# Kernel tuning notes

Measured on AMD Instinct MI355X. Metric: run time of the kernel, lower is better.

Reference implementation:

```python
import jax, jax.numpy as jnp
import numpy as np

B = 8192          # batch of scenes
H = 20            # human_num
O = 10            # other_robot_num
IN = 13           # input_dim
SELF = 6          # self_state_dim
AG = IN - SELF    # agent_state_dim = 7
E1, E2 = 256, 128 # wr_dims / wh_dims
HID = 32          # hardcoded hidden_channels in Graphgnn
FIN = 128         # final_state_dim
P1, P2, P3 = 256, 128, 1  # planning_dims
NE = 8            # number of hetero edge types
# edge-type index convention:
# 0 robot->human, 1 human->robot, 2 other->robot, 3 robot->other,
# 4 other->human, 5 human->other, 6 human->human, 7 other->other


def setup_inputs() -> dict:
    key = jax.random.key(0)
    ks = iter(jax.random.split(key, 40))
    def nrm(shape, scale=0.05):
        return jax.random.normal(next(ks), shape, jnp.float32) * scale
    inp = {}
    inp["state"] = jax.random.normal(next(ks), (B, H + O, IN), jnp.float32)
    inp["dropout"] = 0  # unused by forward (kept for signature fidelity)
    # w_r: SELF -> E1 -> E2 (last_relu=True)
    inp["wr_W0"] = nrm((SELF, E1)); inp["wr_b0"] = nrm((E1,))
    inp["wr_W1"] = nrm((E1, E2));   inp["wr_b1"] = nrm((E2,))
    # w_h: AG -> E1 -> E2
    inp["wh_W0"] = nrm((AG, E1));   inp["wh_b0"] = nrm((E1,))
    inp["wh_W1"] = nrm((E1, E2));   inp["wh_b1"] = nrm((E2,))
    # w_o: AG -> E1 -> E2
    inp["wo_W0"] = nrm((AG, E1));   inp["wo_b0"] = nrm((E1,))
    inp["wo_W1"] = nrm((E1, E2));   inp["wo_b1"] = nrm((E2,))
    # per-edge-type GraphConv params (PyG GraphConv: lin_rel has bias, lin_root has none)
    inp["c1_relW"]  = nrm((NE, E2, HID)); inp["c1_relb"]  = nrm((NE, HID))
    inp["c1_rootW"] = nrm((NE, E2, HID))
    inp["c2_relW"]  = nrm((NE, HID, FIN)); inp["c2_relb"]  = nrm((NE, FIN))
    inp["c2_rootW"] = nrm((NE, HID, FIN))
    # value_net: FIN -> P1 -> P2 -> P3 (no final relu)
    inp["v_W0"] = nrm((FIN, P1)); inp["v_b0"] = nrm((P1,))
    inp["v_W1"] = nrm((P1, P2));  inp["v_b1"] = nrm((P2,))
    inp["v_W2"] = nrm((P2, P3));  inp["v_b2"] = nrm((P3,))
    return inp


def _mlp2(x, W0, b0, W1, b1, last_relu):
    h = jax.nn.relu(x @ W0 + b0)
    h = h @ W1 + b1
    return jax.nn.relu(h) if last_relu else h


def _hetero_conv(xr, xh, xo, relW, relb, rootW):
    # xr: [B,1,D], xh: [B,H,D], xo: [B,O,D]
    # GraphConv per edge type: out_dst = lin_root(x_dst) + lin_rel(sum of src messages)
    # graph is complete bipartite (sence) / complete-minus-self (affect),
    # so aggregations are closed-form sums.
    lin  = lambda x, i: jnp.einsum('bnd,do->bno', x, relW[i]) + relb[i]
    root = lambda x, i: jnp.einsum('bnd,do->bno', x, rootW[i])
    sh = xh.sum(axis=1, keepdims=True)  # [B,1,D] sum over humans
    so = xo.sum(axis=1, keepdims=True)  # [B,1,D] sum over other robots
    # robot receives: human->robot (1), other->robot (2)
    out_r = lin(sh, 1) + root(xr, 1) + lin(so, 2) + root(xr, 2)
    # human receives: robot->human (0), other->human (4), human->human (6)
    out_h = (lin(xr, 0) + root(xh, 0)
             + lin(so, 4) + root(xh, 4)
             + lin(sh - xh, 6) + root(xh, 6))
    # other receives: robot->other (3), human->other (5), other->other (7)
    out_o = (lin(xr, 3) + root(xo, 3)
             + lin(sh, 5) + root(xo, 5)
             + lin(so - xo, 7) + root(xo, 7))
    return out_r, out_h, out_o


def reference(state, dropout,
              wr_W0, wr_b0, wr_W1, wr_b1,
              wh_W0, wh_b0, wh_W1, wh_b1,
              wo_W0, wo_b0, wo_W1, wo_b1,
              c1_relW, c1_relb, c1_rootW,
              c2_relW, c2_relb, c2_rootW,
              v_W0, v_b0, v_W1, v_b1, v_W2, v_b2):
    self_state = state[:, 0, :SELF]          # [B, SELF]
    human_states = state[:, :H, SELF:]       # [B, H, AG]
    other_states = state[:, H:, SELF:]       # [B, O, AG]
    er = _mlp2(self_state, wr_W0, wr_b0, wr_W1, wr_b1, True)[:, None, :]  # [B,1,E2]
    eh = _mlp2(human_states, wh_W0, wh_b0, wh_W1, wh_b1, True)            # [B,H,E2]
    eo = _mlp2(other_states, wo_W0, wo_b0, wo_W1, wo_b1, True)            # [B,O,E2]
    r, h, o = _hetero_conv(er, eh, eo, c1_relW, c1_relb, c1_rootW)
    r, h, o = jax.nn.relu(r), jax.nn.relu(h), jax.nn.relu(o)
    r, h, o = _hetero_conv(r, h, o, c2_relW, c2_relb, c2_rootW)
    r = jax.nn.relu(r)
    hr = r[:, 0, :]                           # robot node per scene, [B, FIN]
    v = jax.nn.relu(hr @ v_W0 + v_b0)
    v = jax.nn.relu(v @ v_W1 + v_b1)
    v = v @ v_W2 + v_b2                       # [B, 1]
    return v
```

## Files before the change

kernel.cpp:

```cpp
#include <hip/hip_runtime.h>
#include <hip/hip_bf16.h>
#include <stdint.h>

#define BATCH 8192
#define NSTATE 30
#define DIN 13
#define E1 256
#define E2 128

typedef short bf16x8 __attribute__((ext_vector_type(8)));
typedef float f32x4 __attribute__((ext_vector_type(4)));

__device__ __forceinline__ unsigned short f2b(float f) {
    unsigned u = __float_as_uint(f);
    u += 0x7FFFu + ((u >> 16) & 1u);
    return (unsigned short)(u >> 16);
}
__device__ __forceinline__ float b2f(unsigned short b) {
    return __uint_as_float((unsigned)b << 16);
}
__device__ __forceinline__ unsigned pack2(float a, float b) {
    return ((unsigned)f2b(fmaxf(b, 0.f)) << 16) | f2b(fmaxf(a, 0.f));
}
__device__ __forceinline__ unsigned pack2n(float a, float b) {
    return ((unsigned)f2b(b) << 16) | f2b(a);
}

__device__ __forceinline__ float wcat_val(int k, int m, const float* relW, const float* rootW) {
    int part = k >> 7, c = k & 127, grp = m >> 5, mm = m & 31;
    int off = c * 32 + mm;
    if (part == 0) return (grp == 0) ? rootW[4096 + off] + rootW[8192 + off]
                        : (grp == 1) ? relW[off] : relW[3*4096 + off];
    if (part == 1) return (grp == 0) ? relW[1*4096 + off]
                        : (grp == 1) ? relW[6*4096 + off] : relW[5*4096 + off];
    return (grp == 0) ? relW[2*4096 + off]
         : (grp == 1) ? relW[4*4096 + off] : relW[7*4096 + off];
}
__device__ __forceinline__ float wc2_val(int k, int n, const float* relW, const float* rootW) {
    int grp = k >> 5, kk = k & 31;
    int off = kk * 128 + n;
    if (grp == 0) return rootW[4096 + off] + rootW[8192 + off];
    if (grp == 1) return relW[4096 + off];
    return relW[8192 + off];
}

__global__ void k_prep(const float* __restrict__ c1_relW, const float* __restrict__ c1_relb,
                       const float* __restrict__ c1_rootW,
                       const float* __restrict__ c2_relW, const float* __restrict__ c2_relb,
                       const float* __restrict__ c2_rootW,
                       const float* __restrict__ wh_W0, const float* __restrict__ wh_W1,
                       const float* __restrict__ wo_W0, const float* __restrict__ wo_W1,
                       const float* __restrict__ wr_W0, const float* __restrict__ wr_W1,
                       const float* __restrict__ v_W0, const float* __restrict__ v_W1,
                       float* __restrict__ bcat, float* __restrict__ bc2,
                       unsigned short* __restrict__ W0b_h, unsigned short* __restrict__ W0b_o,
                       unsigned short* __restrict__ W0b_r,
                       unsigned short* __restrict__ W1f_h, unsigned short* __restrict__ W1f_o,
                       unsigned short* __restrict__ W1f_r,
                       unsigned short* __restrict__ Mf_h, unsigned short* __restrict__ Mf_o,
                       unsigned short* __restrict__ Wcatf, unsigned short* __restrict__ Wc2f,
                       unsigned short* __restrict__ vW0f, unsigned short* __restrict__ vW1f)
{
    int gid = blockIdx.x * blockDim.x + threadIdx.x;
    int gsz = gridDim.x * blockDim.x;

    for (int i = gid; i < 96; i += gsz) {
        int grp = i >> 5, mm = i & 31;
        float v;
        if (grp == 0)      v = c1_relb[32 + mm] + c1_relb[64 + mm];
        else if (grp == 1) v = c1_relb[mm] + c1_relb[128 + mm] + c1_relb[192 + mm];
        else               v = c1_relb[96 + mm] + c1_relb[160 + mm] + c1_relb[224 + mm];
        bcat[i] = v;
    }
    for (int i = gid; i < 128; i += gsz) bc2[i] = c2_relb[128 + i] + c2_relb[256 + i];

    for (int i = gid; i < 2048; i += gsz) {
        int n = i >> 3, j = i & 7;
        W0b_h[i] = (j < 7) ? f2b(wh_W0[j * 256 + n]) : 0;
        W0b_o[i] = (j < 7) ? f2b(wo_W0[j * 256 + n]) : 0;
        W0b_r[i] = (j < 6) ? f2b(wr_W0[j * 256 + n]) : 0;
    }
    for (int i = gid; i < 32768; i += gsz) {
        int j = i & 7, l = (i >> 3) & 63, nt = (i >> 9) & 7, ks = i >> 12;
        int k = ks * 32 + (l >> 4) * 8 + j;
        int n = nt * 16 + (l & 15);
        W1f_h[i] = f2b(wh_W1[k * 128 + n]);
        W1f_o[i] = f2b(wo_W1[k * 128 + n]);
        W1f_r[i] = f2b(wr_W1[k * 128 + n]);
    }
    for (int i = gid; i < 4096; i += gsz) {
        int j = i & 7, l = (i >> 3) & 63, nt = (i >> 9) & 1, ks = i >> 10;
        int k = ks * 32 + (l >> 4) * 8 + j;
        int n = nt * 16 + (l & 15);
        int i0 = k * 32 + n;
        Mf_h[i] = f2b(c1_rootW[i0] + c1_rootW[4*4096 + i0] + c1_rootW[6*4096 + i0] - c1_relW[6*4096 + i0]);
        Mf_o[i] = f2b(c1_rootW[3*4096 + i0] + c1_rootW[5*4096 + i0] + c1_rootW[7*4096 + i0] - c1_relW[7*4096 + i0]);
    }
    for (int i = gid; i < 36864; i += gsz) {
        int j = i & 7, l = (i >> 3) & 63, rem = i >> 9;
        int nt = rem % 6, ks = rem / 6;
        int k = ks * 32 + (l >> 4) * 8 + j;
        int n = nt * 16 + (l & 15);
        Wcatf[i] = f2b(wcat_val(k, n, c1_relW, c1_rootW));
    }
    for (int i = gid; i < 12288; i += gsz) {
        int j = i & 7, l = (i >> 3) & 63, rem = i >> 9;
        int nt = rem & 7, ks = rem >> 3;
        int k = ks * 32 + (l >> 4) * 8 + j;
        int n = nt * 16 + (l & 15);
        Wc2f[i] = f2b(wc2_val(k, n, c2_relW, c2_rootW));
    }
    for (int i = gid; i < 32768; i += gsz) {
        int j = i & 7, l = (i >> 3) & 63, rem = i >> 9;
        int nt = rem & 15, ks = rem >> 4;
        int k = ks * 32 + (l >> 4) * 8 + j;
        int n = nt * 16 + (l & 15);
        vW0f[i] = f2b(v_W0[k * 256 + n]);
    }
    for (int i = gid; i < 32768; i += gsz) {
        int j = i & 7, l = (i >> 3) & 63, rem = i >> 9;
        int nt = rem & 7, ks = rem >> 3;
        int k = ks * 32 + (l >> 4) * 8 + j;
        int n = nt * 16 + (l & 15);
        vW1f[i] = f2b(v_W1[k * 128 + n]);
    }
}

#define SM_W0   0
#define SM_MF   4096
#define SM_W1   12288
#define SM_B0   77824
#define SM_B1   78848
#define SM_HS   79360
#define SM_SZ   (79360 + 8 * 16 * 264 * 2)

template<int NPB, int NODE0, int INOFF, int INDIM, bool TAIL>
__device__ __forceinline__ void mlp_blockE(
    int blkrow0, const float* __restrict__ state,
    const unsigned short* __restrict__ W0b_g, const float* __restrict__ b0,
    const unsigned short* __restrict__ W1f_g, const float* __restrict__ b1,
    const unsigned short* __restrict__ Mf_g,
    unsigned short* __restrict__ tR, float* __restrict__ sumB,
    unsigned short* __restrict__ eR, char* smem)
{
    unsigned short* W0s = (unsigned short*)(smem + SM_W0);
    unsigned short* Mfs = (unsigned short*)(smem + SM_MF);
    unsigned short* W1s = (unsigned short*)(smem + SM_W1);
    float* b0s          = (float*)(smem + SM_B0);
    float* b1s          = (float*)(smem + SM_B1);

    const int t = threadIdx.x;
    const int lane = t & 63;
    const int w = t >> 6;
    const int l15 = lane & 15;
    const int quad = lane >> 4;
    const int R0 = blkrow0 + w * 128;
    unsigned short* hw = (unsigned short*)(smem + SM_HS) + w * (16 * 264);
    unsigned short* ew = hw;

    if (t < 256) { ((uint4*)W0s)[t] = ((const uint4*)W0b_g)[t]; b0s[t] = b0[t]; }
    if (t >= 256 && t < 384) b1s[t - 256] = b1[t - 256];
    #pragma unroll
    for (int i = 0; i < 8; ++i)
        ((uint4*)W1s)[t + 512 * i] = ((const uint4*)W1f_g)[t + 512 * i];
    if constexpr (TAIL)
        ((uint4*)Mfs)[t] = ((const uint4*)Mf_g)[t];
    __syncthreads();

    float s0 = 0.f, s1 = 0.f;
    int bcur = R0 / NPB;

    for (int sub = 0; sub < 8; ++sub) {
        const int wrow0 = R0 + sub * 16;

        bf16x8 bx = {};
        if (quad == 0) {
            int grow = wrow0 + l15;
            int b = grow / NPB;
            int n = grow - b * NPB + NODE0;
            const float* xp = state + ((size_t)b * NSTATE + n) * DIN + INOFF;
            #pragma unroll
            for (int j = 0; j < INDIM; ++j)
                bx[j] = (short)f2b(xp[j]);
        }

        #pragma unroll
        for (int nt = 0; nt < 16; ++nt) {
            bf16x8 aw = {};
            if (quad == 0)
                aw = *(const bf16x8*)(W0s + (nt * 16 + l15) * 8);
            float4 bb = *(const float4*)(b0s + nt * 16 + quad * 4);
            f32x4 c = {bb.x, bb.y, bb.z, bb.w};
            c = __builtin_amdgcn_mfma_f32_16x16x32_bf16(aw, bx, c, 0, 0, 0);
            uint2 pv = {pack2(c[0], c[1]), pack2(c[2], c[3])};
            *(uint2*)(hw + l15 * 264 + nt * 16 + quad * 4) = pv;
        }

        f32x4 acc[8];
        #pragma unroll
        for (int nt = 0; nt < 8; ++nt) {
            float4 bb = *(const float4*)(b1s + nt * 16 + quad * 4);
            acc[nt] = (f32x4){bb.x, bb.y, bb.z, bb.w};
        }
        #pragma unroll
        for (int ks = 0; ks < 8; ++ks) {
            bf16x8 bh = *(const bf16x8*)(hw + l15 * 264 + ks * 32 + quad * 8);
            #pragma unroll
            for (int nt = 0; nt < 8; ++nt) {
                bf16x8 aw = *(const bf16x8*)(W1s + ((ks * 8 + nt) * 64 + lane) * 8);
                acc[nt] = __builtin_amdgcn_mfma_f32_16x16x32_bf16(aw, bh, acc[nt], 0, 0, 0);
            }
        }

        if constexpr (TAIL) {
            __asm__ __volatile__("s_waitcnt lgkmcnt(0)" ::: "memory");
            #pragma unroll
            for (int nt = 0; nt < 8; ++nt) {
                uint2 pv = {pack2(acc[nt][0], acc[nt][1]), pack2(acc[nt][2], acc[nt][3])};
                *(uint2*)(ew + l15 * 136 + nt * 16 + quad * 4) = pv;
            }

            f32x4 tacc[2] = {{0.f,0.f,0.f,0.f},{0.f,0.f,0.f,0.f}};
            #pragma unroll
            for (int ks = 0; ks < 4; ++ks) {
                bf16x8 ae = *(const bf16x8*)(ew + l15 * 136 + ks * 32 + quad * 8);
                #pragma unroll
                for (int nt = 0; nt < 2; ++nt) {
                    bf16x8 bm = *(const bf16x8*)(Mfs + ((ks * 2 + nt) * 64 + lane) * 8);
                    tacc[nt] = __builtin_amdgcn_mfma_f32_16x16x32_bf16(bm, ae, tacc[nt], 0, 0, 0);
                }
            }
            #pragma unroll
            for (int nt = 0; nt < 2; ++nt) {
                uint2 pv = {pack2n(tacc[nt][0], tacc[nt][1]), pack2n(tacc[nt][2], tacc[nt][3])};
                *(uint2*)(tR + (size_t)(wrow0 + l15) * 32 + nt * 16 + quad * 4) = pv;
            }

            #pragma unroll
            for (int r = 0; r < 16; ++r) {
                int b = (wrow0 + r) / NPB;
                if (b != bcur) {
                    bool interior = (bcur * NPB >= R0) && ((bcur + 1) * NPB <= R0 + 128);
                    float* dst = sumB + (size_t)bcur * 128 + 2 * lane;
                    if (interior) { dst[0] = s0; dst[1] = s1; }
                    else { atomicAdd(dst, s0); atomicAdd(dst + 1, s1); }
                    s0 = 0.f; s1 = 0.f; bcur = b;
                }
                unsigned v = *(const unsigned*)(ew + r * 136 + lane * 2);
                s0 += b2f((unsigned short)v);
                s1 += b2f((unsigned short)(v >> 16));
            }
            if (sub == 7) {
                bool interior = (bcur * NPB >= R0) && ((bcur + 1) * NPB <= R0 + 128);
                float* dst = sumB + (size_t)bcur * 128 + 2 * lane;
                if (interior) { dst[0] = s0; dst[1] = s1; }
                else { atomicAdd(dst, s0); atomicAdd(dst + 1, s1); }
            }
        } else {
            #pragma unroll
            for (int nt = 0; nt < 8; ++nt) {
                uint2 pv = {pack2(acc[nt][0], acc[nt][1]), pack2(acc[nt][2], acc[nt][3])};
                *(uint2*)(eR + (size_t)(wrow0 + l15) * 128 + nt * 16 + quad * 4) = pv;
            }
        }
        __asm__ __volatile__("" ::: "memory");
    }
}

__global__ __launch_bounds__(512, 2) void k_mlpE(
    const float* __restrict__ state,
    const unsigned short* __restrict__ W0b_h, const float* __restrict__ b0_h,
    const unsigned short* __restrict__ W1f_h, const float* __restrict__ b1_h,
    const unsigned short* __restrict__ Mf_h, unsigned short* __restrict__ tR_h,
    float* __restrict__ shB,
    const unsigned short* __restrict__ W0b_o, const float* __restrict__ b0_o,
    const unsigned short* __restrict__ W1f_o, const float* __restrict__ b1_o,
    const unsigned short* __restrict__ Mf_o, unsigned short* __restrict__ tR_o,
    float* __restrict__ soB,
    const unsigned short* __restrict__ W0b_r, const float* __restrict__ b0_r,
    const unsigned short* __restrict__ W1f_r, const float* __restrict__ b1_r,
    unsigned short* __restrict__ eR)
{
    __shared__ __align__(16) char smem[SM_SZ];
    int bid = blockIdx.x;
    if (bid < 160)
        mlp_blockE<20, 0, 6, 7, true>(bid * 1024, state, W0b_h, b0_h, W1f_h, b1_h,
                                      Mf_h, tR_h, shB, nullptr, smem);
    else if (bid < 240)
        mlp_blockE<10, 20, 6, 7, true>((bid - 160) * 1024, state, W0b_o, b0_o, W1f_o, b1_o,
                                       Mf_o, tR_o, soB, nullptr, smem);
    else
        mlp_blockE<1, 0, 0, 6, false>((bid - 240) * 1024, state, W0b_r, b0_r, W1f_r, b1_r,
                                      nullptr, nullptr, nullptr, eR, smem);
}

__global__ __launch_bounds__(256, 2) void k_tail(
    const unsigned short* __restrict__ eR,
    const float* __restrict__ shB, const float* __restrict__ soB,
    const unsigned short* __restrict__ tR_h, const unsigned short* __restrict__ tR_o,
    const unsigned short* __restrict__ Wcatf, const float* __restrict__ bcat,
    const unsigned short* __restrict__ Wc2f, const float* __restrict__ bc2,
    const unsigned short* __restrict__ vW0f, const float* __restrict__ vb0,
    const unsigned short* __restrict__ vW1f, const float* __restrict__ vb1,
    const float* __restrict__ vW2, const float* __restrict__ vb2,
    float* __restrict__ out)
{
    __shared__ __align__(16) char sm[33024];
    unsigned short* Ub  = (unsigned short*)(sm);
    unsigned short* V1b = (unsigned short*)(sm);
    unsigned short* Vb  = (unsigned short*)(sm + 12800);
    float* chL          = (float*)(sm + 16128);
    float* coL          = (float*)(sm + 18176);
    unsigned short* Hb  = (unsigned short*)(sm + 20224);
    float* V2b          = (float*)(sm + 24576);

    const int t = threadIdx.x, lane = t & 63, w = t >> 6;
    const int l15 = lane & 15, quad = lane >> 4;
    const int b0 = blockIdx.x * 16;
    const int rowb = quad * 4;

    {
        int b = t >> 4, q = t & 15;
        ((uint4*)(Ub + b * 400))[q] = ((const uint4*)(eR + (size_t)(b0 + b) * 128))[q];
    }
    for (int idx = t; idx < 4096; idx += 256) {
        int b = idx >> 8, kk = idx & 255;
        float v = (kk < 128) ? shB[(size_t)(b0 + b) * 128 + kk]
                             : soB[(size_t)(b0 + b) * 128 + kk - 128];
        Ub[b * 400 + 128 + kk] = f2b(v);
    }
    __syncthreads();

    for (int nt = w; nt < 6; nt += 4) {
        float bias = bcat[nt * 16 + l15];
        f32x4 acc = {bias, bias, bias, bias};
        #pragma unroll
        for (int ks = 0; ks < 12; ++ks) {
            bf16x8 a = *(const bf16x8*)(Ub + l15 * 400 + ks * 32 + quad * 8);
            bf16x8 bw = *(const bf16x8*)(Wcatf + ((ks * 6 + nt) * 64 + lane) * 8);
            acc = __builtin_amdgcn_mfma_f32_16x16x32_bf16(a, bw, acc, 0, 0, 0);
        }
        int n = nt * 16 + l15;
        #pragma unroll
        for (int reg = 0; reg < 4; ++reg) {
            float v = acc[reg];
            int b = rowb + reg;
            if (n < 32)      Vb[b * 104 + n] = f2b(fmaxf(v, 0.f));
            else if (n < 64) chL[b * 32 + (n - 32)] = v;
            else             coL[b * 32 + (n - 64)] = v;
        }
    }
    __syncthreads();

    for (int idx = t; idx < 512; idx += 256) {
        int b = idx >> 5, m = idx & 31;
        float ch = chL[b * 32 + m];
        const unsigned short* p = tR_h + (size_t)(b0 + b) * 20 * 32 + m;
        float s = 0.f;
        #pragma unroll
        for (int n = 0; n < 20; ++n) s += fmaxf(ch + b2f(p[n * 32]), 0.f);
        Vb[b * 104 + 32 + m] = f2b(s);
        float co = coL[b * 32 + m];
        const unsigned short* p2 = tR_o + (size_t)(b0 + b) * 10 * 32 + m;
        float s2 = 0.f;
        #pragma unroll
        for (int n = 0; n < 10; ++n) s2 += fmaxf(co + b2f(p2[n * 32]), 0.f);
        Vb[b * 104 + 64 + m] = f2b(s2);
    }
    __syncthreads();

    {
        f32x4 acc[2];
        #pragma unroll
        for (int q = 0; q < 2; ++q) {
            int nt = w + q * 4;
            float bias = bc2[nt * 16 + l15];
            acc[q] = (f32x4){bias, bias, bias, bias};
        }
        #pragma unroll
        for (int ks = 0; ks < 3; ++ks) {
            bf16x8 a = *(const bf16x8*)(Vb + l15 * 104 + ks * 32 + quad * 8);
            #pragma unroll
            for (int q = 0; q < 2; ++q) {
                int nt = w + q * 4;
                bf16x8 bw = *(const bf16x8*)(Wc2f + ((ks * 8 + nt) * 64 + lane) * 8);
                acc[q] = __builtin_amdgcn_mfma_f32_16x16x32_bf16(a, bw, acc[q], 0, 0, 0);
            }
        }
        #pragma unroll
        for (int q = 0; q < 2; ++q) {
            int nt = w + q * 4;
            #pragma unroll
            for (int reg = 0; reg < 4; ++reg)
                Hb[(rowb + reg) * 136 + nt * 16 + l15] = f2b(fmaxf(acc[q][reg], 0.f));
        }
    }
    __syncthreads();

    {
        f32x4 acc[4];
        #pragma unroll
        for (int q = 0; q < 4; ++q) {
            int nt = w + q * 4;
            float bias = vb0[nt * 16 + l15];
            acc[q] = (f32x4){bias, bias, bias, bias};
        }
        #pragma unroll
        for (int ks = 0; ks < 4; ++ks) {
            bf16x8 a = *(const bf16x8*)(Hb + l15 * 136 + ks * 32 + quad * 8);
            #pragma unroll
            for (int q = 0; q < 4; ++q) {
                int nt = w + q * 4;
                bf16x8 bw = *(const bf16x8*)(vW0f + ((ks * 16 + nt) * 64 + lane) * 8);
                acc[q] = __builtin_amdgcn_mfma_f32_16x16x32_bf16(a, bw, acc[q], 0, 0, 0);
            }
        }
        __syncthreads();
        #pragma unroll
        for (int q = 0; q < 4; ++q) {
            int nt = w + q * 4;
            #pragma unroll
            for (int reg = 0; reg < 4; ++reg)
                V1b[(rowb + reg) * 264 + nt * 16 + l15] = f2b(fmaxf(acc[q][reg], 0.f));
        }
    }
    __syncthreads();

    {
        f32x4 acc[2];
        #pragma unroll
        for (int q = 0; q < 2; ++q) {
            int nt = w + q * 4;
            float bias = vb1[nt * 16 + l15];
            acc[q] = (f32x4){bias, bias, bias, bias};
        }
        #pragma unroll
        for (int ks = 0; ks < 8; ++ks) {
            bf16x8 a = *(const bf16x8*)(V1b + l15 * 264 + ks * 32 + quad * 8);
            #pragma unroll
            for (int q = 0; q < 2; ++q) {
                int nt = w + q * 4;
                bf16x8 bw = *(const bf16x8*)(vW1f + ((ks * 8 + nt) * 64 + lane) * 8);
                acc[q] = __builtin_amdgcn_mfma_f32_16x16x32_bf16(a, bw, acc[q], 0, 0, 0);
            }
        }
        #pragma unroll
        for (int q = 0; q < 2; ++q) {
            int nt = w + q * 4;
            #pragma unroll
            for (int reg = 0; reg < 4; ++reg)
                V2b[(rowb + reg) * 132 + nt * 16 + l15] = fmaxf(acc[q][reg], 0.f);
        }
    }
    __syncthreads();

    if (t < 128) {
        int b = t >> 3, j = t & 7;
        float v = 0.f;
        #pragma unroll
        for (int k = 0; k < 16; ++k)
            v = fmaf(V2b[b * 132 + j * 16 + k], vW2[j * 16 + k], v);
        v += __shfl_down(v, 4, 8);
        v += __shfl_down(v, 2, 8);
        v += __shfl_down(v, 1, 8);
        if (j == 0) out[b0 + b] = v + vb2[0];
    }
}

extern "C" void kernel_launch(void* const* d_in, const int* in_sizes, int n_in,
                              void* d_out, int out_size, void* d_ws, size_t ws_size,
                              hipStream_t stream)
{
    const float* state   = (const float*)d_in[0];
    const float* wr_W0   = (const float*)d_in[2];
    const float* wr_b0   = (const float*)d_in[3];
    const float* wr_W1   = (const float*)d_in[4];
    const float* wr_b1   = (const float*)d_in[5];
    const float* wh_W0   = (const float*)d_in[6];
    const float* wh_b0   = (const float*)d_in[7];
    const float* wh_W1   = (const float*)d_in[8];
    const float* wh_b1   = (const float*)d_in[9];
    const float* wo_W0   = (const float*)d_in[10];
    const float* wo_b0   = (const float*)d_in[11];
    const float* wo_W1   = (const float*)d_in[12];
    const float* wo_b1   = (const float*)d_in[13];
    const float* c1_relW = (const float*)d_in[14];
    const float* c1_relb = (const float*)d_in[15];
    const float* c1_rootW= (const float*)d_in[16];
    const float* c2_relW = (const float*)d_in[17];
    const float* c2_relb = (const float*)d_in[18];
    const float* c2_rootW= (const float*)d_in[19];
    const float* v_W0    = (const float*)d_in[20];
    const float* v_b0    = (const float*)d_in[21];
    const float* v_W1    = (const float*)d_in[22];
    const float* v_b1    = (const float*)d_in[23];
    const float* v_W2    = (const float*)d_in[24];
    const float* v_b2    = (const float*)d_in[25];

    char* ws = (char*)d_ws;
    size_t off = 0;
    auto alloc = [&](size_t bytes) -> char* {
        char* p = ws + off;
        off = (off + bytes + 255) & ~(size_t)255;
        return p;
    };
    float* shB  = (float*)alloc((size_t)BATCH * 128 * 4);
    float* soB  = (float*)alloc((size_t)BATCH * 128 * 4);
    unsigned short* tR_h = (unsigned short*)alloc((size_t)163840 * 32 * 2);
    unsigned short* tR_o = (unsigned short*)alloc((size_t)81920 * 32 * 2);
    unsigned short* eR   = (unsigned short*)alloc((size_t)BATCH * 128 * 2);
    float* bcat = (float*)alloc(96 * 4);
    float* bc2  = (float*)alloc(128 * 4);
    unsigned short* W0b_h = (unsigned short*)alloc(2048 * 2);
    unsigned short* W0b_o = (unsigned short*)alloc(2048 * 2);
    unsigned short* W0b_r = (unsigned short*)alloc(2048 * 2);
    unsigned short* W1f_h = (unsigned short*)alloc(32768 * 2);
    unsigned short* W1f_o = (unsigned short*)alloc(32768 * 2);
    unsigned short* W1f_r = (unsigned short*)alloc(32768 * 2);
    unsigned short* Mf_h  = (unsigned short*)alloc(4096 * 2);
    unsigned short* Mf_o  = (unsigned short*)alloc(4096 * 2);
    unsigned short* Wcatf = (unsigned short*)alloc(36864 * 2);
    unsigned short* Wc2f  = (unsigned short*)alloc(12288 * 2);
    unsigned short* vW0f  = (unsigned short*)alloc(32768 * 2);
    unsigned short* vW1f  = (unsigned short*)alloc(32768 * 2);
    (void)ws_size; (void)in_sizes; (void)n_in; (void)out_size;

    hipMemsetAsync(shB, 0, (size_t)2 * BATCH * 128 * 4, stream);

    k_prep<<<256, 256, 0, stream>>>(c1_relW, c1_relb, c1_rootW, c2_relW, c2_relb, c2_rootW,
                                    wh_W0, wh_W1, wo_W0, wo_W1, wr_W0, wr_W1, v_W0, v_W1,
                                    bcat, bc2, W0b_h, W0b_o, W0b_r, W1f_h, W1f_o, W1f_r,
                                    Mf_h, Mf_o, Wcatf, Wc2f, vW0f, vW1f);

    k_mlpE<<<248, 512, 0, stream>>>(state,
                                    W0b_h, wh_b0, W1f_h, wh_b1, Mf_h, tR_h, shB,
                                    W0b_o, wo_b0, W1f_o, wo_b1, Mf_o, tR_o, soB,
                                    W0b_r, wr_b0, W1f_r, wr_b1, eR);

    k_tail<<<512, 256, 0, stream>>>(eR, shB, soB, tR_h, tR_o,
                                    Wcatf, bcat, Wc2f, bc2, vW0f, v_b0, vW1f, v_b1,
                                    v_W2, v_b2, (float*)d_out);
}
```

Measured before the change: 172.7 us.

## Cache half of W1 in registers, prefetch next input rows, use native bf16 converts

```diff
diff --git a/kernel.cpp b/kernel.cpp
--- a/kernel.cpp
+++ b/kernel.cpp
@@ -10,20 +10,21 @@
 
 typedef short bf16x8 __attribute__((ext_vector_type(8)));
 typedef float f32x4 __attribute__((ext_vector_type(4)));
+typedef __bf16 bf16x2_t __attribute__((ext_vector_type(2)));
 
 __device__ __forceinline__ unsigned short f2b(float f) {
-    unsigned u = __float_as_uint(f);
-    u += 0x7FFFu + ((u >> 16) & 1u);
-    return (unsigned short)(u >> 16);
+    return __builtin_bit_cast(unsigned short, (__bf16)f);
 }
 __device__ __forceinline__ float b2f(unsigned short b) {
     return __uint_as_float((unsigned)b << 16);
 }
 __device__ __forceinline__ unsigned pack2(float a, float b) {
-    return ((unsigned)f2b(fmaxf(b, 0.f)) << 16) | f2b(fmaxf(a, 0.f));
+    bf16x2_t v = {(__bf16)fmaxf(a, 0.f), (__bf16)fmaxf(b, 0.f)};
+    return __builtin_bit_cast(unsigned, v);
 }
 __device__ __forceinline__ unsigned pack2n(float a, float b) {
-    return ((unsigned)f2b(b) << 16) | f2b(a);
+    bf16x2_t v = {(__bf16)a, (__bf16)b};
+    return __builtin_bit_cast(unsigned, v);
 }
 
 __device__ __forceinline__ float wcat_val(int k, int m, const float* relW, const float* rootW) {
@@ -167,21 +168,45 @@
         ((uint4*)Mfs)[t] = ((const uint4*)Mf_g)[t];
     __syncthreads();
 
+    bf16x8 wreg[32];
+    #pragma unroll
+    for (int ks = 0; ks < 8; ++ks)
+        #pragma unroll
+        for (int nt = 0; nt < 4; ++nt)
+            wreg[ks * 4 + nt] = *(const bf16x8*)(W1s + ((ks * 8 + nt) * 64 + lane) * 8);
+
     float s0 = 0.f, s1 = 0.f;
     int bcur = R0 / NPB;
 
-    for (int sub = 0; sub < 8; ++sub) {
-        const int wrow0 = R0 + sub * 16;
-
-        bf16x8 bx = {};
+    float xf[INDIM];
+    #pragma unroll 1
+    for (int dummy = 0; dummy < 1; ++dummy) {
         if (quad == 0) {
-            int grow = wrow0 + l15;
+            int grow = R0 + l15;
             int b = grow / NPB;
             int n = grow - b * NPB + NODE0;
             const float* xp = state + ((size_t)b * NSTATE + n) * DIN + INOFF;
             #pragma unroll
+            for (int j = 0; j < INDIM; ++j) xf[j] = xp[j];
+        }
+    }
+
+    for (int sub = 0; sub < 8; ++sub) {
+        const int wrow0 = R0 + sub * 16;
+
+        bf16x8 bx = {};
+        if (quad == 0) {
+            #pragma unroll
             for (int j = 0; j < INDIM; ++j)
-                bx[j] = (short)f2b(xp[j]);
+                bx[j] = (short)f2b(xf[j]);
+        }
+        if (sub < 7 && quad == 0) {
+            int grow = wrow0 + 16 + l15;
+            int b = grow / NPB;
+            int n = grow - b * NPB + NODE0;
+            const float* xp = state + ((size_t)b * NSTATE + n) * DIN + INOFF;
+            #pragma unroll
+            for (int j = 0; j < INDIM; ++j) xf[j] = xp[j];
         }
 
         #pragma unroll
@@ -207,7 +232,9 @@
             bf16x8 bh = *(const bf16x8*)(hw + l15 * 264 + ks * 32 + quad * 8);
             #pragma unroll
             for (int nt = 0; nt < 8; ++nt) {
-                bf16x8 aw = *(const bf16x8*)(W1s + ((ks * 8 + nt) * 64 + lane) * 8);
+                bf16x8 aw = (nt < 4)
+                    ? wreg[ks * 4 + nt]
+                    : *(const bf16x8*)(W1s + ((ks * 8 + nt) * 64 + lane) * 8);
                 acc[nt] = __builtin_amdgcn_mfma_f32_16x16x32_bf16(aw, bh, acc[nt], 0, 0, 0);
             }
         }
```

Result: faster. 167.2 us (-3.2%).
